# Kernel tuning notes

Measured on AMD Instinct MI355X. Metric: run time of the kernel, lower is better.

Reference implementation:

```python
import jax, jax.numpy as jnp
import numpy as np

B = 16384
L = 128   # l_output_dim
H = 64    # hidden_dim
CTX = 16  # task_ctx_dim
DIMS = [2048, 167, 768, 512, 768, 300]  # RDK, MACCS, MolT5, MolCLR, UniMolV2_84M, GraphMVP
N = len(DIMS)


def setup_inputs() -> dict:
    key = jax.random.key(0)
    ks = jax.random.split(key, 64)
    names = ["x_rdk", "x_maccs", "x_molt5", "x_molclr", "x_unimol", "x_gmvp"]
    inp = {}
    for i, (n, d) in enumerate(zip(names, DIMS)):
        inp[n] = jax.random.normal(ks[i], (B, d), dtype=jnp.float32)
    inp["task_context"] = jax.random.normal(ks[10], (B, CTX), dtype=jnp.float32)
    # per-branch projection Linear(d -> L), stored as [d, L] for x @ W + b
    for i, d in enumerate(DIMS):
        s = 1.0 / np.sqrt(d)
        inp[f"Wp{i}"] = jax.random.uniform(ks[12 + i], (d, L), jnp.float32, -s, s)
        inp[f"bp{i}"] = jax.random.uniform(ks[20 + i], (L,), jnp.float32, -s, s)
    # attention MLP: Linear(L->H), ReLU, Linear(H->1)
    s1 = 1.0 / np.sqrt(L)
    inp["W1"] = jax.random.uniform(ks[30], (L, H), jnp.float32, -s1, s1)
    inp["b1"] = jax.random.uniform(ks[31], (H,), jnp.float32, -s1, s1)
    s2 = 1.0 / np.sqrt(H)
    inp["W2"] = jax.random.uniform(ks[32], (H, 1), jnp.float32, -s2, s2)
    inp["b2"] = jax.random.uniform(ks[33], (1,), jnp.float32, -s2, s2)
    inp["comp_beta"] = jnp.asarray(1.0, dtype=jnp.float32)
    # scalar task gate: Linear(CTX -> N)
    sg = 1.0 / np.sqrt(CTX)
    inp["Wg"] = jax.random.uniform(ks[34], (CTX, N), jnp.float32, -sg, sg)
    inp["bg"] = jax.random.uniform(ks[35], (N,), jnp.float32, -sg, sg)
    return inp


def reference(x_rdk, x_maccs, x_molt5, x_molclr, x_unimol, x_gmvp, task_context,
              Wp0, bp0, Wp1, bp1, Wp2, bp2, Wp3, bp3, Wp4, bp4, Wp5, bp5,
              W1, b1, W2, b2, comp_beta, Wg, bg):
    xs = [x_rdk, x_maccs, x_molt5, x_molclr, x_unimol, x_gmvp]
    Wps = [Wp0, Wp1, Wp2, Wp3, Wp4, Wp5]
    bps = [bp0, bp1, bp2, bp3, bp4, bp5]
    # per-branch projection to L dims
    projs = [x @ W + b for x, W, b in zip(xs, Wps, bps)]
    embeds = jnp.stack(projs, axis=1)  # [B, N, L]
    # validity mask per (sample, branch)
    norms = jnp.linalg.norm(embeds, axis=-1)  # [B, N]
    valid = (~jnp.isnan(embeds).any(axis=-1)) & (norms > 1e-8)  # [B, N]
    # attention MLP score
    h = jax.nn.relu(embeds @ W1 + b1)          # [B, N, H]
    scores = h @ W2 + b2                        # [B, N, 1]
    # cosine complementarity: comp[b, n] = mean_m (1 - cos(proj_n, proj_m))
    normed = embeds / jnp.maximum(norms[..., None], 1e-12)
    cos_sim = jnp.einsum('bnd,bmd->bnm', normed, normed)  # [B, N, N]
    comp_vec = jnp.mean(1.0 - cos_sim, axis=-1, keepdims=True)  # [B, N, 1]
    scores = scores + comp_beta * comp_vec
    # task-aware scalar gate bias
    task_bias = (task_context @ Wg + bg)[:, :, None]  # [B, N, 1]
    scores = scores + task_bias
    # masked softmax over branches
    scores = jnp.where(valid[:, :, None], scores, jnp.float32(-1e9))
    attn_weights = jax.nn.softmax(scores, axis=1)  # [B, N, 1]
    fused = jnp.sum(attn_weights * embeds, axis=1)  # [B, L]
    # dropout is identity (eval mode), sparse_lambda=0 -> sparse_reg omitted
    return fused
```

## Files before the change

### kernel.cpp

```cpp
#include <hip/hip_runtime.h>

typedef _Float16 half8 __attribute__((ext_vector_type(8)));
typedef float    floatx4 __attribute__((ext_vector_type(4)));

#define EMB_BYTES 25165824u

extern "C" __global__ __launch_bounds__(256) void k_prep(
    const float* __restrict__ Wp0, const float* __restrict__ Wp1,
    const float* __restrict__ Wp2, const float* __restrict__ Wp3,
    const float* __restrict__ Wp4, const float* __restrict__ Wp5,
    _Float16* __restrict__ Wt)
{
  const int DPAD_[6] = {2048,192,768,512,768,320};
  int j = blockIdx.x*256 + threadIdx.x;
  int i = 0, st = 0, cum = 0;
  #pragma unroll
  for (int q = 0; q < 6; q++){
    int sz = DPAD_[q] << 4;
    if (j >= cum){ i = q; st = cum; }
    cum += sz;
  }
  int local = j - st;
  int kc = local >> 7;
  int c  = local & 127;
  const float* Wp; int d, dpad, woff;
  switch(i){
    case 0:  Wp=Wp0; d=2048; dpad=2048; woff=0;      break;
    case 1:  Wp=Wp1; d=167;  dpad=192;  woff=262144; break;
    case 2:  Wp=Wp2; d=768;  dpad=768;  woff=286720; break;
    case 3:  Wp=Wp3; d=512;  dpad=512;  woff=385024; break;
    case 4:  Wp=Wp4; d=768;  dpad=768;  woff=450560; break;
    default: Wp=Wp5; d=300;  dpad=320;  woff=548864; break;
  }
  half8 h;
  #pragma unroll
  for (int u = 0; u < 8; u++){
    int k = (kc<<3) + u;
    float v = (k < d) ? Wp[(size_t)k*128 + c] : 0.0f;
    h[u] = (_Float16)v;
  }
  *(half8*)(Wt + woff + (size_t)c*dpad + (kc<<3)) = h;
}

__device__ __forceinline__ void load_a16(const float* __restrict__ xrow,
                                         int kb, int d, bool vec4, float* a)
{
  if (vec4 && (kb + 16 <= d)){
    const float4* p = reinterpret_cast<const float4*>(xrow + kb);
    float4 v0 = p[0], v1 = p[1], v2 = p[2], v3 = p[3];
    a[0]=v0.x;  a[1]=v0.y;  a[2]=v0.z;  a[3]=v0.w;
    a[4]=v1.x;  a[5]=v1.y;  a[6]=v1.z;  a[7]=v1.w;
    a[8]=v2.x;  a[9]=v2.y;  a[10]=v2.z; a[11]=v2.w;
    a[12]=v3.x; a[13]=v3.y; a[14]=v3.z; a[15]=v3.w;
  } else {
    #pragma unroll
    for (int u = 0; u < 16; u++){
      int k = kb + u;
      a[u] = (k < d) ? xrow[k] : 0.0f;
    }
  }
}

__device__ __forceinline__ void cvt_store_a(const float* a, _Float16* dst)
{
  half8 h0, h1;
  #pragma unroll
  for (int u = 0; u < 8; u++){ h0[u] = (_Float16)a[u]; h1[u] = (_Float16)a[8+u]; }
  *(half8*)(dst)     = h0;
  *(half8*)(dst + 8) = h1;
}

extern "C" __global__ __launch_bounds__(256) void k_proj(
    const float* __restrict__ x0, const float* __restrict__ x1,
    const float* __restrict__ x2, const float* __restrict__ x3,
    const float* __restrict__ x4, const float* __restrict__ x5,
    const float* __restrict__ bp0, const float* __restrict__ bp1,
    const float* __restrict__ bp2, const float* __restrict__ bp3,
    const float* __restrict__ bp4, const float* __restrict__ bp5,
    const _Float16* __restrict__ Wt, _Float16* __restrict__ Eo)
{
  __shared__ _Float16 sA[2][128][40];

  int bl = blockIdx.x;
  int slot = bl % 6;
  int mtile = bl / 6;
  const float* x; const float* bp; int i, d, dpad, woff;
  switch(slot){
    case 0:  i=0; x=x0; bp=bp0; d=2048; dpad=2048; woff=0;      break;
    case 1:  i=2; x=x2; bp=bp2; d=768;  dpad=768;  woff=286720; break;
    case 2:  i=4; x=x4; bp=bp4; d=768;  dpad=768;  woff=450560; break;
    case 3:  i=3; x=x3; bp=bp3; d=512;  dpad=512;  woff=385024; break;
    case 4:  i=5; x=x5; bp=bp5; d=300;  dpad=320;  woff=548864; break;
    default: i=1; x=x1; bp=bp1; d=167;  dpad=192;  woff=262144; break;
  }
  int NT = dpad >> 5;
  bool vec4 = ((d & 3) == 0);
  const _Float16* wt = Wt + woff;
  int row0 = mtile << 7;

  int t = threadIdx.x;
  int lane = t & 63, wid = t >> 6;
  int wr = wid >> 1, wc = wid & 1;
  int l15 = lane & 15, l4 = lane >> 4;
  int srow = t >> 1, shalf = t & 1;
  const float* xrow = x + (size_t)(row0 + srow)*d;

  const _Float16* bbase[4];
  #pragma unroll
  for (int nt = 0; nt < 4; nt++)
    bbase[nt] = wt + (size_t)((wc<<6) + (nt<<4) + l15)*dpad + (l4<<3);

  floatx4 acc[4][4];
  #pragma unroll
  for (int a_ = 0; a_ < 4; a_++)
    #pragma unroll
    for (int b_ = 0; b_ < 4; b_++)
      #pragma unroll
      for (int q = 0; q < 4; q++) acc[a_][b_][q] = 0.0f;

  {
    float a0[16];
    load_a16(xrow, (shalf<<4), d, vec4, a0);
    cvt_store_a(a0, &sA[0][srow][shalf<<4]);
  }
  half8 bcur[4];
  #pragma unroll
  for (int nt = 0; nt < 4; nt++) bcur[nt] = *(const half8*)(bbase[nt]);
  __syncthreads();

  for (int kt = 0; kt < NT; kt++){
    int cur = kt & 1;
    bool more = (kt + 1) < NT;
    float anx[16]; half8 bnxt[4];
    if (more){
      load_a16(xrow, ((kt+1)<<5) + (shalf<<4), d, vec4, anx);
      #pragma unroll
      for (int nt = 0; nt < 4; nt++)
        bnxt[nt] = *(const half8*)(bbase[nt] + ((kt+1)<<5));
    }
    #pragma unroll
    for (int mtl = 0; mtl < 4; mtl++){
      half8 af = *(const half8*)&sA[cur][(wr<<6)+(mtl<<4)+l15][l4<<3];
      #pragma unroll
      for (int nt = 0; nt < 4; nt++)
        acc[mtl][nt] = __builtin_amdgcn_mfma_f32_16x16x32_f16(af, bcur[nt], acc[mtl][nt], 0, 0, 0);
    }
    if (more){
      cvt_store_a(anx, &sA[cur^1][srow][shalf<<4]);
      #pragma unroll
      for (int nt = 0; nt < 4; nt++) bcur[nt] = bnxt[nt];
    }
    __syncthreads();
  }

  #pragma unroll
  for (int nt = 0; nt < 4; nt++){
    int col = (wc<<6) + (nt<<4) + l15;
    float bv = bp[col];
    #pragma unroll
    for (int mtl = 0; mtl < 4; mtl++){
      int rbase = row0 + (wr<<6) + (mtl<<4) + (l4<<2);
      #pragma unroll
      for (int j = 0; j < 4; j++){
        float v = acc[mtl][nt][j] + bv;
        Eo[(size_t)(rbase + j)*768 + i*128 + col] = (_Float16)v;
      }
    }
  }
}

extern "C" __global__ __launch_bounds__(256) void k_attn(
    const _Float16* __restrict__ E,
    const float* __restrict__ W1, const float* __restrict__ b1,
    const float* __restrict__ W2, const float* __restrict__ b2,
    const float* __restrict__ beta_,
    const float* __restrict__ Wg, const float* __restrict__ bg,
    const float* __restrict__ ctx, float* __restrict__ out)
{
  __shared__ _Float16 eb[192][136];
  __shared__ _Float16 w1t[64][136];
  __shared__ float s_s1[192];
  __shared__ float s_gate[192];

  int t = threadIdx.x;
  int row0 = blockIdx.x << 5;
  int lane = t & 63, wid = t >> 6;
  int l15 = lane & 15, l4 = lane >> 4;

  {
    const _Float16* src = E + (size_t)row0*768;
    #pragma unroll
    for (int jj = 0; jj < 12; jj++){
      int off8 = t + (jj<<8);
      half8 v = *(const half8*)(src + ((size_t)off8<<3));
      int mrow = off8 >> 4; int kq = off8 & 15;
      *(half8*)&eb[mrow][kq<<3] = v;
    }
    #pragma unroll
    for (int jj = 0; jj < 8; jj++){
      int idx4 = t + (jj<<8);
      float4 v = *(const float4*)(W1 + ((size_t)idx4<<2));
      int k = idx4 >> 4; int h4 = (idx4 & 15) << 2;
      w1t[h4  ][k] = (_Float16)v.x;
      w1t[h4+1][k] = (_Float16)v.y;
      w1t[h4+2][k] = (_Float16)v.z;
      w1t[h4+3][k] = (_Float16)v.w;
    }
    if (t < 192){
      int r = t / 6; int n = t - r*6;
      const float* cr = ctx + (size_t)(row0 + r)*16;
      float g = bg[n];
      #pragma unroll
      for (int k = 0; k < 16; k++) g += cr[k] * Wg[k*6 + n];
      s_gate[t] = g;
    }
  }
  __syncthreads();

  {
    floatx4 acc[3][4];
    #pragma unroll
    for (int a_ = 0; a_ < 3; a_++)
      #pragma unroll
      for (int b_ = 0; b_ < 4; b_++)
        #pragma unroll
        for (int q = 0; q < 4; q++) acc[a_][b_][q] = 0.0f;

    #pragma unroll
    for (int ks = 0; ks < 4; ks++){
      half8 bf[4];
      #pragma unroll
      for (int nt = 0; nt < 4; nt++)
        bf[nt] = *(const half8*)&w1t[(nt<<4)+l15][(ks<<5)+(l4<<3)];
      #pragma unroll
      for (int m3 = 0; m3 < 3; m3++){
        half8 af = *(const half8*)&eb[wid*48 + (m3<<4) + l15][(ks<<5)+(l4<<3)];
        #pragma unroll
        for (int nt = 0; nt < 4; nt++)
          acc[m3][nt] = __builtin_amdgcn_mfma_f32_16x16x32_f16(af, bf[nt], acc[m3][nt], 0, 0, 0);
      }
    }
    float vb1[4], vw2[4];
    #pragma unroll
    for (int nt = 0; nt < 4; nt++){
      int col = (nt<<4) + l15;
      vb1[nt] = b1[col]; vw2[nt] = W2[col];
    }
    float b2v = b2[0];
    #pragma unroll
    for (int m3 = 0; m3 < 3; m3++){
      #pragma unroll
      for (int j = 0; j < 4; j++){
        float p = 0.0f;
        #pragma unroll
        for (int nt = 0; nt < 4; nt++){
          float v = acc[m3][nt][j] + vb1[nt];
          v = fmaxf(v, 0.0f);
          p += v * vw2[nt];
        }
        p += __shfl_xor(p, 1); p += __shfl_xor(p, 2);
        p += __shfl_xor(p, 4); p += __shfl_xor(p, 8);
        if (l15 == 0) s_s1[wid*48 + (m3<<4) + (l4<<2) + j] = p + b2v;
      }
    }
  }
  __syncthreads();

  {
    float BETA = beta_[0];
    for (int rr = 0; rr < 8; rr++){
      int lrow = (wid<<3) + rr;
      float e0[6], e1[6];
      #pragma unroll
      for (int n = 0; n < 6; n++){
        e0[n] = (float)eb[lrow*6+n][lane];
        e1[n] = (float)eb[lrow*6+n][64+lane];
      }
      float red[21];
      int c = 0;
      #pragma unroll
      for (int n = 0; n < 6; n++) red[c++] = e0[n]*e0[n] + e1[n]*e1[n];
      #pragma unroll
      for (int n = 0; n < 6; n++){
        #pragma unroll
        for (int m = n+1; m < 6; m++) red[c++] = e0[n]*e0[m] + e1[n]*e1[m];
      }
      #pragma unroll
      for (int q = 0; q < 21; q++){
        float v = red[q];
        v += __shfl_xor(v, 1);  v += __shfl_xor(v, 2);  v += __shfl_xor(v, 4);
        v += __shfl_xor(v, 8);  v += __shfl_xor(v, 16); v += __shfl_xor(v, 32);
        red[q] = v;
      }
      float den[6]; bool val[6];
      #pragma unroll
      for (int n = 0; n < 6; n++){
        val[n] = red[n] > 1e-16f;
        den[n] = fmaxf(sqrtf(red[n]), 1e-12f);
      }
      float csum[6];
      #pragma unroll
      for (int n = 0; n < 6; n++) csum[n] = red[n] / (den[n]*den[n]);
      {
        int cc = 6;
        #pragma unroll
        for (int n = 0; n < 6; n++){
          #pragma unroll
          for (int m = n+1; m < 6; m++){
            float cv = red[cc++] / (den[n]*den[m]);
            csum[n] += cv; csum[m] += cv;
          }
        }
      }
      float sc[6];
      #pragma unroll
      for (int n = 0; n < 6; n++){
        float comp = 1.0f - csum[n]*(1.0f/6.0f);
        float s = s_s1[lrow*6+n] + BETA*comp + s_gate[lrow*6+n];
        sc[n] = val[n] ? s : -1e9f;
      }
      float mx = sc[0];
      #pragma unroll
      for (int n = 1; n < 6; n++) mx = fmaxf(mx, sc[n]);
      float wsum = 0.0f; float w[6];
      #pragma unroll
      for (int n = 0; n < 6; n++){ w[n] = __expf(sc[n]-mx); wsum += w[n]; }
      float inv = 1.0f / wsum;
      float f0 = 0.0f, f1 = 0.0f;
      #pragma unroll
      for (int n = 0; n < 6; n++){
        float wn = w[n]*inv;
        f0 += wn*e0[n]; f1 += wn*e1[n];
      }
      size_t ob = (size_t)(row0 + lrow)*128;
      out[ob + lane]      = f0;
      out[ob + 64 + lane] = f1;
    }
  }
}

extern "C" void kernel_launch(void* const* d_in, const int* in_sizes, int n_in,
                              void* d_out, int out_size, void* d_ws, size_t ws_size,
                              hipStream_t stream)
{
  const float* x0 = (const float*)d_in[0];
  const float* x1 = (const float*)d_in[1];
  const float* x2 = (const float*)d_in[2];
  const float* x3 = (const float*)d_in[3];
  const float* x4 = (const float*)d_in[4];
  const float* x5 = (const float*)d_in[5];
  const float* ctx = (const float*)d_in[6];
  const float* Wp0 = (const float*)d_in[7];  const float* bp0 = (const float*)d_in[8];
  const float* Wp1 = (const float*)d_in[9];  const float* bp1 = (const float*)d_in[10];
  const float* Wp2 = (const float*)d_in[11]; const float* bp2 = (const float*)d_in[12];
  const float* Wp3 = (const float*)d_in[13]; const float* bp3 = (const float*)d_in[14];
  const float* Wp4 = (const float*)d_in[15]; const float* bp4 = (const float*)d_in[16];
  const float* Wp5 = (const float*)d_in[17]; const float* bp5 = (const float*)d_in[18];
  const float* W1 = (const float*)d_in[19];
  const float* b1 = (const float*)d_in[20];
  const float* W2 = (const float*)d_in[21];
  const float* b2 = (const float*)d_in[22];
  const float* beta = (const float*)d_in[23];
  const float* Wg = (const float*)d_in[24];
  const float* bg = (const float*)d_in[25];

  _Float16* ws_e = (_Float16*)d_ws;
  _Float16* Wt   = (_Float16*)((char*)d_ws + EMB_BYTES);
  float* outp = (float*)d_out;

  k_prep<<<288, 256, 0, stream>>>(Wp0, Wp1, Wp2, Wp3, Wp4, Wp5, Wt);
  k_proj<<<768, 256, 0, stream>>>(x0, x1, x2, x3, x4, x5,
                                  bp0, bp1, bp2, bp3, bp4, bp5, Wt, ws_e);
  k_attn<<<512, 256, 0, stream>>>(ws_e, W1, b1, W2, b2, beta, Wg, bg, ctx, outp);
}
```

Baseline: 441.9 us.

## Halve projection M-tile to 64 rows, raise occupancy, regroup blocks by branch

The projection GEMM tile shrinks from 128 to 64 rows, so each block holds half the accumulators and a smaller shared A buffer, and it requests 5 blocks per CU through launch bounds. The grid doubles to 1536 blocks and is ordered contiguously by branch instead of interleaved. B-fragment register prefetch is dropped in favour of loading B inside each iteration. The aim is more waves in flight to hide latency in this memory-bound projection, at the cost of reading the fp16 weights twice as often and losing explicit B prefetch.

```diff
diff --git a/kernel.cpp b/kernel.cpp
--- a/kernel.cpp
+++ b/kernel.cpp
@@ -42,35 +42,32 @@
   *(half8*)(Wt + woff + (size_t)c*dpad + (kc<<3)) = h;
 }
 
-__device__ __forceinline__ void load_a16(const float* __restrict__ xrow,
-                                         int kb, int d, bool vec4, float* a)
-{
-  if (vec4 && (kb + 16 <= d)){
+__device__ __forceinline__ void load_a8(const float* __restrict__ xrow,
+                                        int kb, int d, bool vec, float* a)
+{
+  if (vec && (kb + 8 <= d)){
     const float4* p = reinterpret_cast<const float4*>(xrow + kb);
-    float4 v0 = p[0], v1 = p[1], v2 = p[2], v3 = p[3];
-    a[0]=v0.x;  a[1]=v0.y;  a[2]=v0.z;  a[3]=v0.w;
-    a[4]=v1.x;  a[5]=v1.y;  a[6]=v1.z;  a[7]=v1.w;
-    a[8]=v2.x;  a[9]=v2.y;  a[10]=v2.z; a[11]=v2.w;
-    a[12]=v3.x; a[13]=v3.y; a[14]=v3.z; a[15]=v3.w;
+    float4 v0 = p[0], v1 = p[1];
+    a[0]=v0.x; a[1]=v0.y; a[2]=v0.z; a[3]=v0.w;
+    a[4]=v1.x; a[5]=v1.y; a[6]=v1.z; a[7]=v1.w;
   } else {
     #pragma unroll
-    for (int u = 0; u < 16; u++){
+    for (int u = 0; u < 8; u++){
       int k = kb + u;
       a[u] = (k < d) ? xrow[k] : 0.0f;
     }
   }
 }
 
-__device__ __forceinline__ void cvt_store_a(const float* a, _Float16* dst)
-{
-  half8 h0, h1;
-  #pragma unroll
-  for (int u = 0; u < 8; u++){ h0[u] = (_Float16)a[u]; h1[u] = (_Float16)a[8+u]; }
-  *(half8*)(dst)     = h0;
-  *(half8*)(dst + 8) = h1;
-}
-
-extern "C" __global__ __launch_bounds__(256) void k_proj(
+__device__ __forceinline__ void cvt_store_a8(const float* a, _Float16* dst)
+{
+  half8 h;
+  #pragma unroll
+  for (int u = 0; u < 8; u++) h[u] = (_Float16)a[u];
+  *(half8*)(dst) = h;
+}
+
+extern "C" __global__ __launch_bounds__(256, 5) void k_proj(
     const float* __restrict__ x0, const float* __restrict__ x1,
     const float* __restrict__ x2, const float* __restrict__ x3,
     const float* __restrict__ x4, const float* __restrict__ x5,
@@ -79,30 +76,37 @@
     const float* __restrict__ bp4, const float* __restrict__ bp5,
     const _Float16* __restrict__ Wt, _Float16* __restrict__ Eo)
 {
-  __shared__ _Float16 sA[2][128][40];
+  __shared__ _Float16 sA[2][64][40];
 
   int bl = blockIdx.x;
-  int slot = bl % 6;
-  int mtile = bl / 6;
-  const float* x; const float* bp; int i, d, dpad, woff;
-  switch(slot){
-    case 0:  i=0; x=x0; bp=bp0; d=2048; dpad=2048; woff=0;      break;
-    case 1:  i=2; x=x2; bp=bp2; d=768;  dpad=768;  woff=286720; break;
-    case 2:  i=4; x=x4; bp=bp4; d=768;  dpad=768;  woff=450560; break;
-    case 3:  i=3; x=x3; bp=bp3; d=512;  dpad=512;  woff=385024; break;
-    case 4:  i=5; x=x5; bp=bp5; d=300;  dpad=320;  woff=548864; break;
-    default: i=1; x=x1; bp=bp1; d=167;  dpad=192;  woff=262144; break;
+  int i, mtile;
+  if      (bl <  256){ i=0; mtile=bl;      }
+  else if (bl <  512){ i=2; mtile=bl-256;  }
+  else if (bl <  768){ i=4; mtile=bl-512;  }
+  else if (bl < 1024){ i=3; mtile=bl-768;  }
+  else if (bl < 1280){ i=5; mtile=bl-1024; }
+  else               { i=1; mtile=bl-1280; }
+
+  const float* x; const float* bp; int d, dpad, woff;
+  switch(i){
+    case 0:  x=x0; bp=bp0; d=2048; dpad=2048; woff=0;      break;
+    case 1:  x=x1; bp=bp1; d=167;  dpad=192;  woff=262144; break;
+    case 2:  x=x2; bp=bp2; d=768;  dpad=768;  woff=286720; break;
+    case 3:  x=x3; bp=bp3; d=512;  dpad=512;  woff=385024; break;
+    case 4:  x=x4; bp=bp4; d=768;  dpad=768;  woff=450560; break;
+    default: x=x5; bp=bp5; d=300;  dpad=320;  woff=548864; break;
   }
   int NT = dpad >> 5;
-  bool vec4 = ((d & 3) == 0);
+  bool vec = ((d & 3) == 0);
   const _Float16* wt = Wt + woff;
-  int row0 = mtile << 7;
+  int row0 = mtile << 6;
 
   int t = threadIdx.x;
   int lane = t & 63, wid = t >> 6;
   int wr = wid >> 1, wc = wid & 1;
   int l15 = lane & 15, l4 = lane >> 4;
-  int srow = t >> 1, shalf = t & 1;
+  int srow = t >> 2;
+  int koff = (t & 3) << 3;
   const float* xrow = x + (size_t)(row0 + srow)*d;
 
   const _Float16* bbase[4];
@@ -110,46 +114,38 @@
   for (int nt = 0; nt < 4; nt++)
     bbase[nt] = wt + (size_t)((wc<<6) + (nt<<4) + l15)*dpad + (l4<<3);
 
-  floatx4 acc[4][4];
-  #pragma unroll
-  for (int a_ = 0; a_ < 4; a_++)
+  floatx4 acc[2][4];
+  #pragma unroll
+  for (int a_ = 0; a_ < 2; a_++)
     #pragma unroll
     for (int b_ = 0; b_ < 4; b_++)
       #pragma unroll
       for (int q = 0; q < 4; q++) acc[a_][b_][q] = 0.0f;
 
   {
-    float a0[16];
-    load_a16(xrow, (shalf<<4), d, vec4, a0);
-    cvt_store_a(a0, &sA[0][srow][shalf<<4]);
-  }
-  half8 bcur[4];
-  #pragma unroll
-  for (int nt = 0; nt < 4; nt++) bcur[nt] = *(const half8*)(bbase[nt]);
+    float a0[8];
+    load_a8(xrow, koff, d, vec, a0);
+    cvt_store_a8(a0, &sA[0][srow][koff]);
+  }
   __syncthreads();
 
   for (int kt = 0; kt < NT; kt++){
     int cur = kt & 1;
     bool more = (kt + 1) < NT;
-    float anx[16]; half8 bnxt[4];
-    if (more){
-      load_a16(xrow, ((kt+1)<<5) + (shalf<<4), d, vec4, anx);
+    float anx[8];
+    if (more) load_a8(xrow, ((kt+1)<<5) + koff, d, vec, anx);
+    half8 bf[4];
+    #pragma unroll
+    for (int nt = 0; nt < 4; nt++)
+      bf[nt] = *(const half8*)(bbase[nt] + (kt<<5));
+    #pragma unroll
+    for (int mtl = 0; mtl < 2; mtl++){
+      half8 af = *(const half8*)&sA[cur][(wr<<5)+(mtl<<4)+l15][l4<<3];
       #pragma unroll
       for (int nt = 0; nt < 4; nt++)
-        bnxt[nt] = *(const half8*)(bbase[nt] + ((kt+1)<<5));
-    }
-    #pragma unroll
-    for (int mtl = 0; mtl < 4; mtl++){
-      half8 af = *(const half8*)&sA[cur][(wr<<6)+(mtl<<4)+l15][l4<<3];
-      #pragma unroll
-      for (int nt = 0; nt < 4; nt++)
-        acc[mtl][nt] = __builtin_amdgcn_mfma_f32_16x16x32_f16(af, bcur[nt], acc[mtl][nt], 0, 0, 0);
-    }
-    if (more){
-      cvt_store_a(anx, &sA[cur^1][srow][shalf<<4]);
-      #pragma unroll
-      for (int nt = 0; nt < 4; nt++) bcur[nt] = bnxt[nt];
-    }
+        acc[mtl][nt] = __builtin_amdgcn_mfma_f32_16x16x32_f16(af, bf[nt], acc[mtl][nt], 0, 0, 0);
+    }
+    if (more) cvt_store_a8(anx, &sA[cur^1][srow][koff]);
     __syncthreads();
   }
 
@@ -158,8 +154,8 @@
     int col = (wc<<6) + (nt<<4) + l15;
     float bv = bp[col];
     #pragma unroll
-    for (int mtl = 0; mtl < 4; mtl++){
-      int rbase = row0 + (wr<<6) + (mtl<<4) + (l4<<2);
+    for (int mtl = 0; mtl < 2; mtl++){
+      int rbase = row0 + (wr<<5) + (mtl<<4) + (l4<<2);
       #pragma unroll
       for (int j = 0; j < 4; j++){
         float v = acc[mtl][nt][j] + bv;
@@ -369,7 +365,7 @@
   float* outp = (float*)d_out;
 
   k_prep<<<288, 256, 0, stream>>>(Wp0, Wp1, Wp2, Wp3, Wp4, Wp5, Wt);
-  k_proj<<<768, 256, 0, stream>>>(x0, x1, x2, x3, x4, x5,
-                                  bp0, bp1, bp2, bp3, bp4, bp5, Wt, ws_e);
+  k_proj<<<1536, 256, 0, stream>>>(x0, x1, x2, x3, x4, x5,
+                                   bp0, bp1, bp2, bp3, bp4, bp5, Wt, ws_e);
   k_attn<<<512, 256, 0, stream>>>(ws_e, W1, b1, W2, b2, beta, Wg, bg, ctx, outp);
 }
```

Measured after the change: 445.7 us. Within noise of the previous version (+0.8%).
